# Kernel optimization log

Hardware: AMD Instinct MI355X
Metric: run time of the kernel (lower is better)

Reference implementation:

```python
import jax, jax.numpy as jnp
import numpy as np

B, N, D, S, H = 128, 4096, 64, 7, 128  # batch, tokens, slot_size, num_slots, mlp_hidden
EPS = 1e-8
LN_EPS = 1e-5


def _ln(x, w, b):
    m = jnp.mean(x, axis=-1, keepdims=True)
    v = jnp.mean((x - m) ** 2, axis=-1, keepdims=True)
    return (x - m) * jax.lax.rsqrt(v + LN_EPS) * w + b


def setup_inputs() -> dict:
    key = jax.random.key(0)
    ks = jax.random.split(key, 12)
    glorot = lambda k, shape: jax.random.normal(k, shape, jnp.float32) * (2.0 / sum(shape)) ** 0.5
    return {
        "inputs": jax.random.normal(ks[0], (B, N, D), jnp.float32),
        "slots_noise": jax.random.normal(ks[1], (B, S, D), jnp.float32),
        "ln_in_w": jnp.ones((D,), jnp.float32), "ln_in_b": jnp.zeros((D,), jnp.float32),
        "ln_slots_w": jnp.ones((D,), jnp.float32), "ln_slots_b": jnp.zeros((D,), jnp.float32),
        "ln_mlp_w": jnp.ones((D,), jnp.float32), "ln_mlp_b": jnp.zeros((D,), jnp.float32),
        "slots_mu": jax.random.normal(ks[2], (1, 1, D), jnp.float32),
        "slots_log_sigma": jax.random.normal(ks[3], (1, 1, D), jnp.float32) * 0.1,
        "Wq": glorot(ks[4], (D, D)), "Wk": glorot(ks[5], (D, D)), "Wv": glorot(ks[6], (D, D)),
        "W_ih": glorot(ks[7], (3 * D, D)), "W_hh": glorot(ks[8], (3 * D, D)),
        "b_ih": jnp.zeros((3 * D,), jnp.float32), "b_hh": jnp.zeros((3 * D,), jnp.float32),
        "mlp_W1": glorot(ks[9], (H, D)), "mlp_b1": jnp.zeros((H,), jnp.float32),
        "mlp_W2": glorot(ks[10], (D, H)), "mlp_b2": jnp.zeros((D,), jnp.float32),
        "num_iterations": 3,
    }


def reference(inputs, slots_noise, ln_in_w, ln_in_b, ln_slots_w, ln_slots_b,
              ln_mlp_w, ln_mlp_b, slots_mu, slots_log_sigma, Wq, Wk, Wv,
              W_ih, W_hh, b_ih, b_hh, mlp_W1, mlp_b1, mlp_W2, mlp_b2,
              num_iterations):
    d = inputs.shape[-1]
    x = _ln(inputs, ln_in_w, ln_in_b)            # [B,N,D]
    k = x @ Wk.T                                  # [B,N,D]
    v = x @ Wv.T                                  # [B,N,D]
    slots = slots_mu + jnp.exp(slots_log_sigma) * slots_noise  # [B,S,D]
    scale = d ** -0.5
    for _ in range(num_iterations):
        slots_prev = slots
        s = _ln(slots, ln_slots_w, ln_slots_b)
        q = (s @ Wq.T) * scale                    # [B,S,D]
        logits = jnp.einsum('bnd,bsd->bns', k, q) # [B,N,S]
        attn = jax.nn.softmax(logits, axis=-1) + EPS   # softmax over slots
        attn = attn / jnp.sum(attn, axis=-2, keepdims=True)  # renorm over tokens
        updates = jnp.einsum('bns,bnd->bsd', attn, v)  # [B,S,D]
        # GRUCell (torch semantics)
        gi = updates @ W_ih.T + b_ih              # [B,S,3D]
        gh = slots_prev @ W_hh.T + b_hh
        i_r, i_z, i_n = jnp.split(gi, 3, axis=-1)
        h_r, h_z, h_n = jnp.split(gh, 3, axis=-1)
        r = jax.nn.sigmoid(i_r + h_r)
        z = jax.nn.sigmoid(i_z + h_z)
        n = jnp.tanh(i_n + r * h_n)
        slots = (1.0 - z) * n + z * slots_prev
        m = _ln(slots, ln_mlp_w, ln_mlp_b)
        slots = slots + (jax.nn.relu(m @ mlp_W1.T + mlp_b1) @ mlp_W2.T + mlp_b2)
    return slots
```

## Files before the change

### kernel.cpp

```cpp
#include <hip/hip_runtime.h>


#define Nn 4096

typedef _Float16 f16;
typedef _Float16 f16x8 __attribute__((ext_vector_type(8)));
typedef _Float16 f16x4 __attribute__((ext_vector_type(4)));
typedef float    f32x4 __attribute__((ext_vector_type(4)));

#define MFMA16(a,b,c) __builtin_amdgcn_mfma_f32_16x16x16f16(a,b,c,0,0,0)
#define MFMA32(a,b,c) __builtin_amdgcn_mfma_f32_16x16x32_f16(a,b,c,0,0,0)
#define LGKM0() asm volatile("s_waitcnt lgkmcnt(0)" ::: "memory")

static __device__ __forceinline__ float dot4(f32x4 a, f32x4 b) {
  return a.x*b.x + a.y*b.y + a.z*b.z + a.w*b.w;
}

__global__ __launch_bounds__(256) void k_init(
    const float* __restrict__ noise, const float* __restrict__ mu,
    const float* __restrict__ ls, const float* __restrict__ Wq,
    const float* __restrict__ Wk, float* __restrict__ slots,
    float* __restrict__ Mt)
{
  int bk = blockIdx.x, t = threadIdx.x;
  if (bk < 56) {
    int i = bk*1024 + t*4;
    int d = i & 63;
    f32x4 nz = *(const f32x4*)(noise + i);
    f32x4 m4 = *(const f32x4*)(mu + d);
    f32x4 l4 = *(const f32x4*)(ls + d);
    f32x4 o;
    o.x = m4.x + expf(l4.x)*nz.x; o.y = m4.y + expf(l4.y)*nz.y;
    o.z = m4.z + expf(l4.z)*nz.z; o.w = m4.w + expf(l4.w)*nz.w;
    *(f32x4*)(slots + i) = o;
  } else {
    int idx = (bk-56)*256 + t;
    int d = idx >> 6, e = idx & 63;
    float a = 0.f;
    for (int dd = 0; dd < 64; dd++)
      a += Wk[dd*64 + d] * Wq[dd*64 + e];
    Mt[idx] = a * 0.125f;
  }
}

static __device__ __forceinline__ void stage_chunk(
    float (*Wl)[68], const float* __restrict__ src, int stride, int t)
{
  __syncthreads();
  int r = t >> 2, c4 = (t & 3) * 16;
  #pragma unroll
  for (int k = 0; k < 4; k++)
    *(f32x4*)&Wl[r][c4 + k*4] = *(const f32x4*)(src + (size_t)r*stride + c4 + k*4);
  __syncthreads();
}

static __device__ __forceinline__ float dot_row(
    float (*Wl)[68], int d, const float* v)
{
  float a = 0.f;
  #pragma unroll
  for (int jc = 0; jc < 16; jc++)
    a += dot4(*(const f32x4*)&Wl[d][jc*4], *(const f32x4*)(v + jc*4));
  return a;
}

__global__ __launch_bounds__(256) void k_gru(
    const float* __restrict__ part, const float* __restrict__ csp,
    const float* __restrict__ lnw_in, const float* __restrict__ lnb_in,
    const float* __restrict__ Wv,
    const float* __restrict__ W_ih, const float* __restrict__ W_hh,
    const float* __restrict__ b_ih, const float* __restrict__ b_hh,
    const float* __restrict__ lnm_w, const float* __restrict__ lnm_b,
    const float* __restrict__ W1, const float* __restrict__ b1,
    const float* __restrict__ W2, const float* __restrict__ b2,
    const float* __restrict__ lns_w, const float* __restrict__ lns_b,
    const float* __restrict__ Mt,
    float* __restrict__ slots, f16* __restrict__ qkpad,
    float* __restrict__ qkaux, int do_gru, int do_q)
{
  __shared__ __align__(16) float Wl[64][68];
  __shared__ __align__(16) float updv[4][64];
  __shared__ __align__(16) float u2v [4][64];
  __shared__ __align__(16) float prevv[4][64];
  __shared__ __align__(16) float mlnv[4][64];
  __shared__ __align__(16) float sn2 [4][64];
  __shared__ __align__(16) float hbuf[4][128];
  const int t = threadIdx.x, w = t >> 6, d = t & 63;
  const int wid = blockIdx.x*4 + w;
  const int b = wid / 7, s = wid - b*7;

  float out;
  if (do_gru) {
    float Y = 0.f, alpha = 0.f, delta = 0.f;
    #pragma unroll
    for (int cx = 0; cx < 8; cx++) {
      Y     += part[(((size_t)b*8+cx)*8 + s)*64 + d];
      alpha += csp [(((size_t)b*8+cx)*8 + s)*2 + 0];
      delta += csp [(((size_t)b*8+cx)*8 + s)*2 + 1];
    }
    float upd_pre = lnw_in[d]*(Y - delta)/alpha + lnb_in[d];
    float prev = slots[(size_t)wid*64 + d];
    updv[w][d] = upd_pre; prevv[w][d] = prev;
    LGKM0();

    stage_chunk(Wl, Wv, 64, t);
    u2v[w][d] = dot_row(Wl, d, updv[w]);
    LGKM0();

    stage_chunk(Wl, W_ih,         64, t);
    float air = b_ih[d]     + dot_row(Wl, d, u2v[w]);
    stage_chunk(Wl, W_ih + 4096,  64, t);
    float aiz = b_ih[64+d]  + dot_row(Wl, d, u2v[w]);
    stage_chunk(Wl, W_ih + 8192,  64, t);
    float ain = b_ih[128+d] + dot_row(Wl, d, u2v[w]);
    stage_chunk(Wl, W_hh,         64, t);
    float ahr = b_hh[d]     + dot_row(Wl, d, prevv[w]);
    stage_chunk(Wl, W_hh + 4096,  64, t);
    float ahz = b_hh[64+d]  + dot_row(Wl, d, prevv[w]);
    stage_chunk(Wl, W_hh + 8192,  64, t);
    float ahn = b_hh[128+d] + dot_row(Wl, d, prevv[w]);

    float r = 1.f/(1.f + __expf(-(air+ahr)));
    float z = 1.f/(1.f + __expf(-(aiz+ahz)));
    float n = tanhf(ain + r*ahn);
    float hnew = (1.f - z)*n + z*prev;

    float s1 = hnew, s2 = hnew*hnew;
    #pragma unroll
    for (int m = 1; m < 64; m <<= 1) {
      s1 += __shfl_xor(s1, m, 64);
      s2 += __shfl_xor(s2, m, 64);
    }
    float mean = s1*(1.f/64.f), var = s2*(1.f/64.f) - mean*mean;
    float mln = (hnew - mean) * rsqrtf(var + 1e-5f) * lnm_w[d] + lnm_b[d];
    mlnv[w][d] = mln;
    LGKM0();

    stage_chunk(Wl, W1,        64, t);
    float h0 = fmaxf(b1[d]    + dot_row(Wl, d, mlnv[w]), 0.f);
    stage_chunk(Wl, W1 + 4096, 64, t);
    float h1 = fmaxf(b1[64+d] + dot_row(Wl, d, mlnv[w]), 0.f);
    hbuf[w][d] = h0; hbuf[w][64+d] = h1;
    LGKM0();

    stage_chunk(Wl, W2,      128, t);
    out = hnew + b2[d] + dot_row(Wl, d, hbuf[w]);
    stage_chunk(Wl, W2 + 64, 128, t);
    out += dot_row(Wl, d, hbuf[w] + 64);
    slots[(size_t)wid*64 + d] = out;
  } else {
    out = slots[(size_t)wid*64 + d];
  }

  if (do_q) {
    float s1 = out, s2 = out*out;
    #pragma unroll
    for (int m = 1; m < 64; m <<= 1) {
      s1 += __shfl_xor(s1, m, 64);
      s2 += __shfl_xor(s2, m, 64);
    }
    float mean = s1*(1.f/64.f), var = s2*(1.f/64.f) - mean*mean;
    float sv = (out - mean) * rsqrtf(var + 1e-5f) * lns_w[d] + lns_b[d];
    sn2[w][d] = sv;
    LGKM0();

    stage_chunk(Wl, Mt, 64, t);
    float qk = dot_row(Wl, d, sn2[w]);

    float qw = qk * lnw_in[d];
    float bb = qk * lnb_in[d];
    float gg = qw;
    #pragma unroll
    for (int m = 1; m < 64; m <<= 1) {
      bb += __shfl_xor(bb, m, 64);
      gg += __shfl_xor(gg, m, 64);
    }
    qkpad[((size_t)b*16 + s)*64 + d] = (f16)qw;
    if (d == 0) {
      qkaux[((size_t)b*16 + s)*2 + 0] = bb;
      qkaux[((size_t)b*16 + s)*2 + 1] = gg;
    }
  }
}

__global__ __launch_bounds__(256, 4) void k_attn(
    const float* __restrict__ x_in, const f16* __restrict__ qkpad,
    const float* __restrict__ qkaux,
    float* __restrict__ part, float* __restrict__ csp)
{
  __shared__ __align__(16) float accb[4][8][64];
  __shared__ float ldsc[4][8][2];
  const int b = blockIdx.y, cx = blockIdx.x;
  const int tid = threadIdx.x;
  const int w = tid >> 6, lane = tid & 63, q = lane >> 4, c = lane & 15;

  f16x8 qkB[2];
  qkB[0] = *(const f16x8*)(qkpad + ((size_t)b*16 + c)*64 + q*8);
  qkB[1] = *(const f16x8*)(qkpad + ((size_t)b*16 + c)*64 + 32 + q*8);
  const float beta  = qkaux[((size_t)b*16 + c)*2 + 0];
  const float gamma = qkaux[((size_t)b*16 + c)*2 + 1];

  f16x8 selLo, selHi;
  #pragma unroll
  for (int j = 0; j < 8; j++) {
    selLo[j] = (f16)((( c>>3)    == q && (c&7) == j) ? 1.0f : 0.0f);
    selHi[j] = (f16)(((c>>3) + 2 == q && (c&7) == j) ? 1.0f : 0.0f);
  }

  const f32x4 zero4 = {0.f,0.f,0.f,0.f};
  f32x4 acc[4] = {zero4, zero4, zero4, zero4};
  float csump = 0.f, dsump = 0.f;
  const size_t tok0 = (size_t)b*Nn + (size_t)cx*512 + (size_t)w*128;
  const bool valid = (c < 7);

  f32x4 nx[4];
  {
    const float* base = x_in + (tok0 + c)*64;
    nx[0] = *(const f32x4*)(base + q*8);
    nx[1] = *(const f32x4*)(base + q*8 + 4);
    nx[2] = *(const f32x4*)(base + 32 + q*8);
    nx[3] = *(const f32x4*)(base + 32 + q*8 + 4);
  }

  #pragma unroll
  for (int t = 0; t < 8; t++) {
    f32x4 xv[4];
    #pragma unroll
    for (int i = 0; i < 4; i++) xv[i] = nx[i];
    if (t < 7) {
      const float* base = x_in + (tok0 + (t+1)*16 + c)*64;
      nx[0] = *(const f32x4*)(base + q*8);
      nx[1] = *(const f32x4*)(base + q*8 + 4);
      nx[2] = *(const f32x4*)(base + 32 + q*8);
      nx[3] = *(const f32x4*)(base + 32 + q*8 + 4);
    }
    float sx  = (xv[0].x+xv[0].y+xv[0].z+xv[0].w) + (xv[1].x+xv[1].y+xv[1].z+xv[1].w)
              + (xv[2].x+xv[2].y+xv[2].z+xv[2].w) + (xv[3].x+xv[3].y+xv[3].z+xv[3].w);
    float sxx = dot4(xv[0],xv[0]) + dot4(xv[1],xv[1])
              + dot4(xv[2],xv[2]) + dot4(xv[3],xv[3]);
    sx  += __shfl_xor(sx, 16, 64);  sx  += __shfl_xor(sx, 32, 64);
    sxx += __shfl_xor(sxx, 16, 64); sxx += __shfl_xor(sxx, 32, 64);
    float mean = sx*(1.f/64.f);
    float rstd = rsqrtf(sxx*(1.f/64.f) - mean*mean + 1e-5f);
    float mr = mean * rstd;
    float rT[4], mT[4];
    #pragma unroll
    for (int j = 0; j < 4; j++) {
      rT[j] = __shfl(rstd, q*4 + j, 64);
      mT[j] = __shfl(mr,   q*4 + j, 64);
    }
    f16x8 xf0, xf1;
    #pragma unroll
    for (int j = 0; j < 4; j++) {
      xf0[j] = (f16)xv[0][j]; xf0[4+j] = (f16)xv[1][j];
      xf1[j] = (f16)xv[2][j]; xf1[4+j] = (f16)xv[3][j];
    }
    f32x4 lg = zero4;
    lg = MFMA32(xf0, qkB[0], lg);
    lg = MFMA32(xf1, qkB[1], lg);
    float e[4], sm[4];
    #pragma unroll
    for (int j = 0; j < 4; j++) {
      float L = rT[j]*lg[j] + beta - mT[j]*gamma;
      e[j] = valid ? __expf(L) : 0.f;
      sm[j] = e[j];
    }
    #pragma unroll
    for (int m = 1; m < 16; m <<= 1)
      #pragma unroll
      for (int j = 0; j < 4; j++) sm[j] += __shfl_xor(sm[j], m, 64);
    f16x4 pp;
    #pragma unroll
    for (int j = 0; j < 4; j++) {
      float p = valid ? (e[j]/sm[j] + 1e-8f) : 0.f;
      csump += p;
      dsump += p * mT[j];
      pp[j] = (f16)(p * rT[j]);
    }
    #pragma unroll
    for (int nb = 0; nb < 4; nb++) {
      f32x4 tr = MFMA32(nb < 2 ? xf0 : xf1, (nb & 1) ? selHi : selLo, zero4);
      f16x4 xt; xt.x=(f16)tr.x; xt.y=(f16)tr.y; xt.z=(f16)tr.z; xt.w=(f16)tr.w;
      acc[nb] = MFMA16(pp, xt, acc[nb]);
    }
  }

  csump += __shfl_xor(csump, 16, 64); csump += __shfl_xor(csump, 32, 64);
  dsump += __shfl_xor(dsump, 16, 64); dsump += __shfl_xor(dsump, 32, 64);
  if (q == 0 && c < 7) { ldsc[w][c][0] = csump; ldsc[w][c][1] = dsump; }
  if (q < 2) {
    #pragma unroll
    for (int nb = 0; nb < 4; nb++)
      #pragma unroll
      for (int r = 0; r < 4; r++)
        accb[w][q*4 + r][nb*16 + c] = acc[nb][r];
  }
  __syncthreads();
  for (int rr = tid; rr < 448; rr += 256) {
    int row = rr >> 6, dd = rr & 63;
    float v = accb[0][row][dd] + accb[1][row][dd]
            + accb[2][row][dd] + accb[3][row][dd];
    part[(((size_t)b*8 + cx)*8 + row)*64 + dd] = v;
  }
  if (tid < 14) {
    int s = tid >> 1, k = tid & 1;
    csp[(((size_t)b*8 + cx)*8 + s)*2 + k] =
        ldsc[0][s][k] + ldsc[1][s][k] + ldsc[2][s][k] + ldsc[3][s][k];
  }
}

extern "C" void kernel_launch(void* const* d_in, const int* in_sizes, int n_in,
                              void* d_out, int out_size, void* d_ws, size_t ws_size,
                              hipStream_t stream) {
  const float* inputs  = (const float*)d_in[0];
  const float* noise   = (const float*)d_in[1];
  const float* ln_in_w = (const float*)d_in[2];
  const float* ln_in_b = (const float*)d_in[3];
  const float* ln_sl_w = (const float*)d_in[4];
  const float* ln_sl_b = (const float*)d_in[5];
  const float* ln_ml_w = (const float*)d_in[6];
  const float* ln_ml_b = (const float*)d_in[7];
  const float* mu   = (const float*)d_in[8];
  const float* ls   = (const float*)d_in[9];
  const float* Wq   = (const float*)d_in[10];
  const float* Wk   = (const float*)d_in[11];
  const float* Wv   = (const float*)d_in[12];
  const float* W_ih = (const float*)d_in[13];
  const float* W_hh = (const float*)d_in[14];
  const float* b_ih = (const float*)d_in[15];
  const float* b_hh = (const float*)d_in[16];
  const float* W1 = (const float*)d_in[17];
  const float* b1 = (const float*)d_in[18];
  const float* W2 = (const float*)d_in[19];
  const float* b2 = (const float*)d_in[20];

  float* slots = (float*)d_out;

  const size_t PART_OFF = 0;
  const size_t CSP_OFF  = PART_OFF + 2097152;
  const size_t QK_OFF   = CSP_OFF  + 65536;
  const size_t QA_OFF   = QK_OFF   + 262144;
  const size_t MT_OFF   = QA_OFF   + 16384;
  const size_t NEED     = MT_OFF   + 16384;
  if (ws_size < NEED) return;

  char* ws = (char*)d_ws;
  float* part  = (float*)(ws + PART_OFF);
  float* csp   = (float*)(ws + CSP_OFF);
  f16*   qkpad = (f16*)  (ws + QK_OFF);
  float* qkaux = (float*)(ws + QA_OFF);
  float* Mt    = (float*)(ws + MT_OFF);

  k_init<<<72, 256, 0, stream>>>(noise, mu, ls, Wq, Wk, slots, Mt);
  k_gru<<<224, 256, 0, stream>>>(part, csp, ln_in_w, ln_in_b, Wv,
                                 W_ih, W_hh, b_ih, b_hh, ln_ml_w, ln_ml_b,
                                 W1, b1, W2, b2, ln_sl_w, ln_sl_b, Mt,
                                 slots, qkpad, qkaux, 0, 1);
  dim3 ga(8, 128);
  for (int it = 0; it < 3; it++) {
    k_attn<<<ga, 256, 0, stream>>>(inputs, qkpad, qkaux, part, csp);
    k_gru<<<224, 256, 0, stream>>>(part, csp, ln_in_w, ln_in_b, Wv,
                                   W_ih, W_hh, b_ih, b_hh, ln_ml_w, ln_ml_b,
                                   W1, b1, W2, b2, ln_sl_w, ln_sl_b, Mt,
                                   slots, qkpad, qkaux, 1, it < 2 ? 1 : 0);
  }
}
```

Before: 360.5 us.

## Cache normalized fp16 inputs after first attention pass and simplify LN algebra

On the first attention iteration the kernel layer-normalizes the fp32 inputs, converts them to fp16 and writes them to a 64MB workspace buffer. Later iterations read this half-size fp16 copy, skipping the LN statistics and the fp32 loads. Because the normalized values are now stored, the rstd/mean correction terms (gamma, delta) are dropped from the logits and accumulators, and the softmax divide becomes a reciprocal. The first pass pays extra write traffic and applies the normalization before the fp16 cast, which may shift numerics slightly.

```diff
diff --git a/kernel.cpp b/kernel.cpp
--- a/kernel.cpp
+++ b/kernel.cpp
@@ -11,6 +11,12 @@
 #define MFMA16(a,b,c) __builtin_amdgcn_mfma_f32_16x16x16f16(a,b,c,0,0,0)
 #define MFMA32(a,b,c) __builtin_amdgcn_mfma_f32_16x16x32_f16(a,b,c,0,0,0)
 #define LGKM0() asm volatile("s_waitcnt lgkmcnt(0)" ::: "memory")
+
+#if __has_builtin(__builtin_amdgcn_rcpf)
+#define RCPF(x) __builtin_amdgcn_rcpf(x)
+#else
+#define RCPF(x) (1.0f/(x))
+#endif
 
 static __device__ __forceinline__ float dot4(f32x4 a, f32x4 b) {
   return a.x*b.x + a.y*b.y + a.z*b.z + a.w*b.w;
@@ -91,14 +97,13 @@
 
   float out;
   if (do_gru) {
-    float Y = 0.f, alpha = 0.f, delta = 0.f;
+    float Y = 0.f, alpha = 0.f;
     #pragma unroll
     for (int cx = 0; cx < 8; cx++) {
       Y     += part[(((size_t)b*8+cx)*8 + s)*64 + d];
-      alpha += csp [(((size_t)b*8+cx)*8 + s)*2 + 0];
-      delta += csp [(((size_t)b*8+cx)*8 + s)*2 + 1];
-    }
-    float upd_pre = lnw_in[d]*(Y - delta)/alpha + lnb_in[d];
+      alpha += csp [(((size_t)b*8+cx)*8 + s)];
+    }
+    float upd_pre = lnw_in[d]*(Y/alpha) + lnb_in[d];
     float prev = slots[(size_t)wid*64 + d];
     updv[w][d] = upd_pre; prevv[w][d] = prev;
     LGKM0();
@@ -169,27 +174,55 @@
 
     float qw = qk * lnw_in[d];
     float bb = qk * lnb_in[d];
-    float gg = qw;
-    #pragma unroll
-    for (int m = 1; m < 64; m <<= 1) {
+    #pragma unroll
+    for (int m = 1; m < 64; m <<= 1)
       bb += __shfl_xor(bb, m, 64);
-      gg += __shfl_xor(gg, m, 64);
-    }
     qkpad[((size_t)b*16 + s)*64 + d] = (f16)qw;
-    if (d == 0) {
-      qkaux[((size_t)b*16 + s)*2 + 0] = bb;
-      qkaux[((size_t)b*16 + s)*2 + 1] = gg;
-    }
+    if (d == 0) qkaux[(size_t)b*16 + s] = bb;
+  }
+}
+
+static __device__ __forceinline__ void tile_common(
+    f16x8 xf0, f16x8 xf1, const f16x8* qkB, float beta,
+    f16x8 selLo, f16x8 selHi, bool valid, f32x4* acc, float& csump)
+{
+  const f32x4 zero4 = {0.f,0.f,0.f,0.f};
+  f32x4 lg = zero4;
+  lg = MFMA32(xf0, qkB[0], lg);
+  lg = MFMA32(xf1, qkB[1], lg);
+  float e[4], sm[4];
+  #pragma unroll
+  for (int j = 0; j < 4; j++) {
+    float L = lg[j] + beta;
+    e[j] = valid ? __expf(L) : 0.f;
+    sm[j] = e[j];
+  }
+  #pragma unroll
+  for (int m = 1; m < 16; m <<= 1)
+    #pragma unroll
+    for (int j = 0; j < 4; j++) sm[j] += __shfl_xor(sm[j], m, 64);
+  f16x4 pp;
+  #pragma unroll
+  for (int j = 0; j < 4; j++) {
+    float p = valid ? (e[j]*RCPF(sm[j]) + 1e-8f) : 0.f;
+    csump += p;
+    pp[j] = (f16)p;
+  }
+  #pragma unroll
+  for (int nb = 0; nb < 4; nb++) {
+    f32x4 tr = MFMA32(nb < 2 ? xf0 : xf1, (nb & 1) ? selHi : selLo, zero4);
+    f16x4 xt; xt.x=(f16)tr.x; xt.y=(f16)tr.y; xt.z=(f16)tr.z; xt.w=(f16)tr.w;
+    acc[nb] = MFMA16(pp, xt, acc[nb]);
   }
 }
 
 __global__ __launch_bounds__(256, 4) void k_attn(
     const float* __restrict__ x_in, const f16* __restrict__ qkpad,
-    const float* __restrict__ qkaux,
-    float* __restrict__ part, float* __restrict__ csp)
+    const float* __restrict__ qkaux, f16* __restrict__ xh,
+    float* __restrict__ part, float* __restrict__ csp, int first)
 {
   __shared__ __align__(16) float accb[4][8][64];
-  __shared__ float ldsc[4][8][2];
+  __shared__ float ldsc[4][8];
   const int b = blockIdx.y, cx = blockIdx.x;
   const int tid = threadIdx.x;
   const int w = tid >> 6, lane = tid & 63, q = lane >> 4, c = lane & 15;
@@ -197,8 +230,7 @@
   f16x8 qkB[2];
   qkB[0] = *(const f16x8*)(qkpad + ((size_t)b*16 + c)*64 + q*8);
   qkB[1] = *(const f16x8*)(qkpad + ((size_t)b*16 + c)*64 + 32 + q*8);
-  const float beta  = qkaux[((size_t)b*16 + c)*2 + 0];
-  const float gamma = qkaux[((size_t)b*16 + c)*2 + 1];
+  const float beta = qkaux[(size_t)b*16 + c];
 
   f16x8 selLo, selHi;
   #pragma unroll
@@ -209,85 +241,75 @@
 
   const f32x4 zero4 = {0.f,0.f,0.f,0.f};
   f32x4 acc[4] = {zero4, zero4, zero4, zero4};
-  float csump = 0.f, dsump = 0.f;
+  float csump = 0.f;
   const size_t tok0 = (size_t)b*Nn + (size_t)cx*512 + (size_t)w*128;
   const bool valid = (c < 7);
 
-  f32x4 nx[4];
-  {
-    const float* base = x_in + (tok0 + c)*64;
-    nx[0] = *(const f32x4*)(base + q*8);
-    nx[1] = *(const f32x4*)(base + q*8 + 4);
-    nx[2] = *(const f32x4*)(base + 32 + q*8);
-    nx[3] = *(const f32x4*)(base + 32 + q*8 + 4);
-  }
-
-  #pragma unroll
-  for (int t = 0; t < 8; t++) {
-    f32x4 xv[4];
-    #pragma unroll
-    for (int i = 0; i < 4; i++) xv[i] = nx[i];
-    if (t < 7) {
-      const float* base = x_in + (tok0 + (t+1)*16 + c)*64;
+  if (first) {
+    f32x4 nx[4];
+    {
+      const float* base = x_in + (tok0 + c)*64;
       nx[0] = *(const f32x4*)(base + q*8);
       nx[1] = *(const f32x4*)(base + q*8 + 4);
       nx[2] = *(const f32x4*)(base + 32 + q*8);
       nx[3] = *(const f32x4*)(base + 32 + q*8 + 4);
     }
-    float sx  = (xv[0].x+xv[0].y+xv[0].z+xv[0].w) + (xv[1].x+xv[1].y+xv[1].z+xv[1].w)
-              + (xv[2].x+xv[2].y+xv[2].z+xv[2].w) + (xv[3].x+xv[3].y+xv[3].z+xv[3].w);
-    float sxx = dot4(xv[0],xv[0]) + dot4(xv[1],xv[1])
-              + dot4(xv[2],xv[2]) + dot4(xv[3],xv[3]);
-    sx  += __shfl_xor(sx, 16, 64);  sx  += __shfl_xor(sx, 32, 64);
-    sxx += __shfl_xor(sxx, 16, 64); sxx += __shfl_xor(sxx, 32, 64);
-    float mean = sx*(1.f/64.f);
-    float rstd = rsqrtf(sxx*(1.f/64.f) - mean*mean + 1e-5f);
-    float mr = mean * rstd;
-    float rT[4], mT[4];
-    #pragma unroll
-    for (int j = 0; j < 4; j++) {
-      rT[j] = __shfl(rstd, q*4 + j, 64);
-      mT[j] = __shfl(mr,   q*4 + j, 64);
-    }
-    f16x8 xf0, xf1;
-    #pragma unroll
-    for (int j = 0; j < 4; j++) {
-      xf0[j] = (f16)xv[0][j]; xf0[4+j] = (f16)xv[1][j];
-      xf1[j] = (f16)xv[2][j]; xf1[4+j] = (f16)xv[3][j];
-    }
-    f32x4 lg = zero4;
-    lg = MFMA32(xf0, qkB[0], lg);
-    lg = MFMA32(xf1, qkB[1], lg);
-    float e[4], sm[4];
-    #pragma unroll
-    for (int j = 0; j < 4; j++) {
-      float L = rT[j]*lg[j] + beta - mT[j]*gamma;
-      e[j] = valid ? __expf(L) : 0.f;
-      sm[j] = e[j];
-    }
-    #pragma unroll
-    for (int m = 1; m < 16; m <<= 1)
+    #pragma unroll
+    for (int t = 0; t < 8; t++) {
+      f32x4 xv[4];
       #pragma unroll
-      for (int j = 0; j < 4; j++) sm[j] += __shfl_xor(sm[j], m, 64);
-    f16x4 pp;
-    #pragma unroll
-    for (int j = 0; j < 4; j++) {
-      float p = valid ? (e[j]/sm[j] + 1e-8f) : 0.f;
-      csump += p;
-      dsump += p * mT[j];
-      pp[j] = (f16)(p * rT[j]);
-    }
-    #pragma unroll
-    for (int nb = 0; nb < 4; nb++) {
-      f32x4 tr = MFMA32(nb < 2 ? xf0 : xf1, (nb & 1) ? selHi : selLo, zero4);
-      f16x4 xt; xt.x=(f16)tr.x; xt.y=(f16)tr.y; xt.z=(f16)tr.z; xt.w=(f16)tr.w;
-      acc[nb] = MFMA16(pp, xt, acc[nb]);
+      for (int i = 0; i < 4; i++) xv[i] = nx[i];
+      if (t < 7) {
+        const float* base = x_in + (tok0 + (t+1)*16 + c)*64;
+        nx[0] = *(const f32x4*)(base + q*8);
+        nx[1] = *(const f32x4*)(base + q*8 + 4);
+        nx[2] = *(const f32x4*)(base + 32 + q*8);
+        nx[3] = *(const f32x4*)(base + 32 + q*8 + 4);
+      }
+      float sx  = (xv[0].x+xv[0].y+xv[0].z+xv[0].w) + (xv[1].x+xv[1].y+xv[1].z+xv[1].w)
+                + (xv[2].x+xv[2].y+xv[2].z+xv[2].w) + (xv[3].x+xv[3].y+xv[3].z+xv[3].w);
+      float sxx = dot4(xv[0],xv[0]) + dot4(xv[1],xv[1])
+                + dot4(xv[2],xv[2]) + dot4(xv[3],xv[3]);
+      sx  += __shfl_xor(sx, 16, 64);  sx  += __shfl_xor(sx, 32, 64);
+      sxx += __shfl_xor(sxx, 16, 64); sxx += __shfl_xor(sxx, 32, 64);
+      float mean = sx*(1.f/64.f);
+      float rstd = rsqrtf(sxx*(1.f/64.f) - mean*mean + 1e-5f);
+      float mr2 = mean * rstd;
+      f16x8 xf0, xf1;
+      #pragma unroll
+      for (int j = 0; j < 4; j++) {
+        xf0[j]   = (f16)(xv[0][j]*rstd - mr2);
+        xf0[4+j] = (f16)(xv[1][j]*rstd - mr2);
+        xf1[j]   = (f16)(xv[2][j]*rstd - mr2);
+        xf1[4+j] = (f16)(xv[3][j]*rstd - mr2);
+      }
+      f16* xo = xh + (tok0 + t*16 + c)*64;
+      *(f16x8*)(xo + q*8)      = xf0;
+      *(f16x8*)(xo + 32 + q*8) = xf1;
+
+      tile_common(xf0, xf1, qkB, beta, selLo, selHi, valid, acc, csump);
+    }
+  } else {
+    f16x8 n0, n1;
+    {
+      const f16* base = xh + (tok0 + c)*64;
+      n0 = *(const f16x8*)(base + q*8);
+      n1 = *(const f16x8*)(base + 32 + q*8);
+    }
+    #pragma unroll
+    for (int t = 0; t < 8; t++) {
+      f16x8 xf0 = n0, xf1 = n1;
+      if (t < 7) {
+        const f16* base = xh + (tok0 + (t+1)*16 + c)*64;
+        n0 = *(const f16x8*)(base + q*8);
+        n1 = *(const f16x8*)(base + 32 + q*8);
+      }
+      tile_common(xf0, xf1, qkB, beta, selLo, selHi, valid, acc, csump);
     }
   }
 
   csump += __shfl_xor(csump, 16, 64); csump += __shfl_xor(csump, 32, 64);
-  dsump += __shfl_xor(dsump, 16, 64); dsump += __shfl_xor(dsump, 32, 64);
-  if (q == 0 && c < 7) { ldsc[w][c][0] = csump; ldsc[w][c][1] = dsump; }
+  if (q == 0 && c < 7) ldsc[w][c] = csump;
   if (q < 2) {
     #pragma unroll
     for (int nb = 0; nb < 4; nb++)
@@ -302,10 +324,9 @@
             + accb[2][row][dd] + accb[3][row][dd];
     part[(((size_t)b*8 + cx)*8 + row)*64 + dd] = v;
   }
-  if (tid < 14) {
-    int s = tid >> 1, k = tid & 1;
-    csp[(((size_t)b*8 + cx)*8 + s)*2 + k] =
-        ldsc[0][s][k] + ldsc[1][s][k] + ldsc[2][s][k] + ldsc[3][s][k];
+  if (tid < 7) {
+    csp[(((size_t)b*8 + cx)*8 + tid)] =
+        ldsc[0][tid] + ldsc[1][tid] + ldsc[2][tid] + ldsc[3][tid];
   }
 }
 
@@ -338,10 +359,11 @@
 
   const size_t PART_OFF = 0;
   const size_t CSP_OFF  = PART_OFF + 2097152;
-  const size_t QK_OFF   = CSP_OFF  + 65536;
+  const size_t QK_OFF   = CSP_OFF  + 32768;
   const size_t QA_OFF   = QK_OFF   + 262144;
-  const size_t MT_OFF   = QA_OFF   + 16384;
-  const size_t NEED     = MT_OFF   + 16384;
+  const size_t MT_OFF   = QA_OFF   + 8192;
+  const size_t XH_OFF   = MT_OFF   + 16384;
+  const size_t NEED     = XH_OFF   + 67108864;
   if (ws_size < NEED) return;
 
   char* ws = (char*)d_ws;
@@ -350,6 +372,7 @@
   f16*   qkpad = (f16*)  (ws + QK_OFF);
   float* qkaux = (float*)(ws + QA_OFF);
   float* Mt    = (float*)(ws + MT_OFF);
+  f16*   xh    = (f16*)  (ws + XH_OFF);
 
   k_init<<<72, 256, 0, stream>>>(noise, mu, ls, Wq, Wk, slots, Mt);
   k_gru<<<224, 256, 0, stream>>>(part, csp, ln_in_w, ln_in_b, Wv,
@@ -358,7 +381,8 @@
                                  slots, qkpad, qkaux, 0, 1);
   dim3 ga(8, 128);
   for (int it = 0; it < 3; it++) {
-    k_attn<<<ga, 256, 0, stream>>>(inputs, qkpad, qkaux, part, csp);
+    k_attn<<<ga, 256, 0, stream>>>(inputs, qkpad, qkaux, xh, part, csp,
+                                   it == 0 ? 1 : 0);
     k_gru<<<224, 256, 0, stream>>>(part, csp, ln_in_w, ln_in_b, Wv,
                                    W_ih, W_hh, b_ih, b_hh, ln_ml_w, ln_ml_b,
                                    W1, b1, W2, b2, ln_sl_w, ln_sl_b, Mt,
```

After: 322.3 us. 1.12x faster.
